# Optimization experiments

Measured on AMD Instinct MI355X. Metric: run time of the kernel, lower is better.

## Reference

```python
import jax, jax.numpy as jnp
import numpy as np

B, N, E, H, ID = 32, 256, 512, 8, 8
D = E // H  # head dim = 64


def setup_inputs() -> dict:
    key = jax.random.key(0)
    ks = jax.random.split(key, 6)
    s = lambda k, shape, fan_in: jax.random.normal(k, shape, jnp.float32) * (fan_in ** -0.5)
    return {
        "x": jax.random.normal(ks[0], (B, N, E), jnp.float32),
        "U": jax.random.normal(ks[1], (B, N, N, ID), jnp.float32),
        "w_qkv": s(ks[2], (3 * E, E), E),   # nn.MultiheadAttention in_proj_weight
        "b_qkv": jnp.zeros((3 * E,), jnp.float32),
        "w_out": s(ks[3], (E, E), E),       # out_proj.weight
        "b_out": jnp.zeros((E,), jnp.float32),
        "w_u": s(ks[4], (H, ID), ID),       # u_proj.weight
        "b_u": jnp.zeros((H,), jnp.float32),
    }


def reference(x, U, w_qkv, b_qkv, w_out, b_out, w_u, b_u):
    # fused QKV projection (torch MHA uses a single in_proj)
    qkv = x @ w_qkv.T + b_qkv                      # [B,N,3E]
    q, k, v = jnp.split(qkv, 3, axis=-1)
    split_heads = lambda t: t.reshape(B, N, H, D).transpose(0, 2, 1, 3)  # [B,H,N,D]
    q, k, v = split_heads(q), split_heads(k), split_heads(v)
    # interaction tensor -> one additive bias per head: [B,N,N,H] -> [B,H,N,N]
    bias = (U @ w_u.T + b_u).transpose(0, 3, 1, 2)
    logits = jnp.einsum('bhnd,bhmd->bhnm', q, k) * (D ** -0.5) + bias  # [B,H,N,N]
    attn = jax.nn.softmax(logits, axis=-1)
    o = jnp.einsum('bhnm,bhmd->bhnd', attn, v)     # [B,H,N,D]
    o = o.transpose(0, 2, 1, 3).reshape(B, N, E)
    return o @ w_out.T + b_out
```

## Files before the change

### kernel.cpp

```cpp
#include <hip/hip_runtime.h>
#include <stdint.h>

#define Bn 32
#define Nn 256
#define En 512
#define Hn 8
#define Dn 64

typedef __attribute__((ext_vector_type(8))) short bf16x8;
typedef __attribute__((ext_vector_type(4))) short bf16x4;
typedef __attribute__((ext_vector_type(4))) float f32x4;
typedef __attribute__((ext_vector_type(4))) _Float16 h4f;

__device__ __forceinline__ unsigned short f2bf(float f){
  union{float f; uint32_t i;} v; v.f = f;
  uint32_t i = v.i;
  return (unsigned short)((i + 0x7fffu + ((i>>16)&1u)) >> 16);
}

__device__ __forceinline__ void stage16(const unsigned short* g,
                                        unsigned short* lds_wave_base,
                                        unsigned short* lds_lane){
#if __has_builtin(__builtin_amdgcn_global_load_lds)
  __builtin_amdgcn_global_load_lds(
      (const __attribute__((address_space(1))) unsigned int*)g,
      (__attribute__((address_space(3))) unsigned int*)lds_wave_base, 16, 0, 0);
  (void)lds_lane;
#else
  *(bf16x8*)lds_lane = *(const bf16x8*)g;
  (void)lds_wave_base;
#endif
}

__global__ __launch_bounds__(256) void convert_x(
    const float* __restrict__ x, unsigned short* __restrict__ xb){
  size_t i = ((size_t)blockIdx.x * 256 + threadIdx.x) * 8;
  float4 a = *(const float4*)(x + i);
  float4 b = *(const float4*)(x + i + 4);
  bf16x8 p;
  p[0]=(short)f2bf(a.x); p[1]=(short)f2bf(a.y); p[2]=(short)f2bf(a.z); p[3]=(short)f2bf(a.w);
  p[4]=(short)f2bf(b.x); p[5]=(short)f2bf(b.y); p[6]=(short)f2bf(b.z); p[7]=(short)f2bf(b.w);
  *(bf16x8*)(xb + i) = p;
}

__global__ __launch_bounds__(256) void prep_kernel(
    const float* __restrict__ x, unsigned short* __restrict__ xb,
    const float* __restrict__ U, const float* __restrict__ w_u,
    const float* __restrict__ b_u, unsigned short* __restrict__ bias16,
    const float* __restrict__ wq, unsigned short* __restrict__ wqb,
    const float* __restrict__ wo, unsigned short* __restrict__ wob){
  __shared__ float s_wu[64];
  __shared__ float s_bu[8];
  const int bx = blockIdx.x;
  const int tid = threadIdx.x;
  if (bx < 2048 || bx >= 4096) {
    const float* src; unsigned short* dst; size_t i;
    if (bx < 2048)      { src = x;  dst = xb;  i = ((size_t)bx * 256 + tid) * 8; }
    else if (bx < 4480) { src = wq; dst = wqb; i = ((size_t)(bx-4096) * 256 + tid) * 8; }
    else                { src = wo; dst = wob; i = ((size_t)(bx-4480) * 256 + tid) * 8; }
    float4 a = *(const float4*)(src + i);
    float4 b = *(const float4*)(src + i + 4);
    bf16x8 p;
    p[0]=(short)f2bf(a.x); p[1]=(short)f2bf(a.y); p[2]=(short)f2bf(a.z); p[3]=(short)f2bf(a.w);
    p[4]=(short)f2bf(b.x); p[5]=(short)f2bf(b.y); p[6]=(short)f2bf(b.z); p[7]=(short)f2bf(b.w);
    *(bf16x8*)(dst + i) = p;
    return;
  }
  if (tid < 64) s_wu[tid] = w_u[tid];
  if (tid < 8)  s_bu[tid] = b_u[tid];
  __syncthreads();
  const int t  = (bx - 2048) * 256 + tid;
  const int m_ = t & 255;
  const int n4 = (t >> 8) & 63;
  const int bb = t >> 14;
  const float* up = U + ((size_t)(bb*Nn + n4*4)*Nn + m_) * 8;
  float u[4][8];
  #pragma unroll
  for (int r = 0; r < 4; ++r) {
    float4 a = *(const float4*)(up + (size_t)r * (Nn*8));
    float4 c = *(const float4*)(up + (size_t)r * (Nn*8) + 4);
    u[r][0]=a.x; u[r][1]=a.y; u[r][2]=a.z; u[r][3]=a.w;
    u[r][4]=c.x; u[r][5]=c.y; u[r][6]=c.z; u[r][7]=c.w;
  }
  const int    lane_in = ((n4 & 3) * 16 + (m_ & 15)) * 4;
  const size_t tbase   = ((size_t)(n4 >> 2) * 16 + (m_ >> 4)) * 256;
  #pragma unroll
  for (int h = 0; h < 8; ++h) {
    const float bu = s_bu[h];
    float acc[4];
    #pragma unroll
    for (int r = 0; r < 4; ++r) {
      float a = bu;
      #pragma unroll
      for (int id = 0; id < 8; ++id) a += u[r][id] * s_wu[h*8 + id];
      acc[r] = a;
    }
    h4f hv;
    hv[0]=(_Float16)acc[0]; hv[1]=(_Float16)acc[1];
    hv[2]=(_Float16)acc[2]; hv[3]=(_Float16)acc[3];
    *(h4f*)(bias16 + (size_t)(bb*Hn + h) * 65536 + tbase + lane_in) = hv;
  }
}

__global__ __launch_bounds__(256) void qkv_gemm3(
    const unsigned short* __restrict__ xb, const unsigned short* __restrict__ wqb,
    const float* __restrict__ bq,
    unsigned short* __restrict__ q_ws, unsigned short* __restrict__ k_ws,
    unsigned short* __restrict__ v_ws){
  __shared__ unsigned short s_a[2][128*64];
  __shared__ unsigned short s_b[2][128*64];
  const int tid = threadIdx.x;
  const int bx = blockIdx.x;
  const int by = blockIdx.y;
  const int row0 = by * 128, n0 = bx * 128;
  const int lane = tid & 63, wv = tid >> 6;
  const int wr = wv >> 1, wc = wv & 1;
  const int lm = lane & 15, quad = lane >> 4;
  f32x4 acc[4][4] = {};

  auto stage_tile = [&](int buf, int kc){
    const int k0 = kc * 64;
    #pragma unroll
    for (int i = 0; i < 4; ++i) {
      const int ci = i*256 + tid;
      const int r = ci >> 3, c = ci & 7;
      const int sc = (c ^ (r & 7)) * 8;
      stage16(xb  + (size_t)(row0 + r)*512 + k0 + sc,
              s_a[buf] + (size_t)(i*256 + wv*64)*8, s_a[buf] + (size_t)ci*8);
      stage16(wqb + (size_t)(n0  + r)*512 + k0 + sc,
              s_b[buf] + (size_t)(i*256 + wv*64)*8, s_b[buf] + (size_t)ci*8);
    }
  };

  stage_tile(0, 0);
  __syncthreads();
  #pragma unroll 1
  for (int kc = 0; kc < 8; ++kc) {
    const int cur = kc & 1;
    if (kc + 1 < 8) stage_tile(cur ^ 1, kc + 1);
    #pragma unroll
    for (int ks = 0; ks < 2; ++ks) {
      bf16x8 af[4], bfr[4];
      #pragma unroll
      for (int mt = 0; mt < 4; ++mt) {
        const int r = wr*64 + mt*16 + lm;
        af[mt] = *(const bf16x8*)(s_a[cur] + (size_t)r*64 + (((ks*4 + quad) ^ (r & 7)) * 8));
      }
      #pragma unroll
      for (int nt = 0; nt < 4; ++nt) {
        const int r = wc*64 + nt*16 + lm;
        bfr[nt] = *(const bf16x8*)(s_b[cur] + (size_t)r*64 + (((ks*4 + quad) ^ (r & 7)) * 8));
      }
      #pragma unroll
      for (int mt = 0; mt < 4; ++mt)
        #pragma unroll
        for (int nt = 0; nt < 4; ++nt)
          acc[mt][nt] = __builtin_amdgcn_mfma_f32_16x16x32_bf16(af[mt], bfr[nt], acc[mt][nt], 0, 0, 0);
    }
    __syncthreads();
  }
  #pragma unroll
  for (int nt = 0; nt < 4; ++nt) {
    int c = n0 + wc*64 + nt*16 + lm;
    float bias = bq[c];
    int sec = c >> 9, ch = c & 511, h = ch >> 6, d = ch & 63;
    #pragma unroll
    for (int mt = 0; mt < 4; ++mt) {
      #pragma unroll
      for (int r = 0; r < 4; ++r) {
        int grow = row0 + wr*64 + mt*16 + quad*4 + r;
        int b = grow >> 8, n = grow & 255;
        float val = acc[mt][nt][r] + bias;
        if (sec == 0)      q_ws[(((size_t)b*Hn + h)*Nn + n)*Dn + d] = f2bf(val * 0.125f);
        else if (sec == 1) k_ws[(((size_t)b*Hn + h)*Nn + n)*Dn + d] = f2bf(val);
        else               v_ws[(((size_t)b*Hn + h)*Dn + d)*Nn + n] = f2bf(val);
      }
    }
  }
}

__global__ __launch_bounds__(256) void oproj_gemm3(
    const unsigned short* __restrict__ o_ws, const unsigned short* __restrict__ wob,
    const float* __restrict__ bo, float* __restrict__ out){
  __shared__ unsigned short s_a[2][128*64];
  __shared__ unsigned short s_b[2][64*64];
  const int tid = threadIdx.x;
  const int bx = blockIdx.x;
  const int by = blockIdx.y;
  const int row0 = by * 128, n0 = bx * 64;
  const int lane = tid & 63, wv = tid >> 6;
  const int wr = wv >> 1, wc = wv & 1;
  const int lm = lane & 15, quad = lane >> 4;
  f32x4 acc[4][2] = {};

  auto stage_tile = [&](int buf, int kc){
    const int k0 = kc * 64;
    #pragma unroll
    for (int i = 0; i < 4; ++i) {
      const int ci = i*256 + tid;
      const int r = ci >> 3, c = ci & 7;
      const int sc = (c ^ (r & 7)) * 8;
      stage16(o_ws + (size_t)(row0 + r)*512 + k0 + sc,
              s_a[buf] + (size_t)(i*256 + wv*64)*8, s_a[buf] + (size_t)ci*8);
    }
    #pragma unroll
    for (int i = 0; i < 2; ++i) {
      const int ci = i*256 + tid;
      const int r = ci >> 3, c = ci & 7;
      const int sc = (c ^ (r & 7)) * 8;
      stage16(wob + (size_t)(n0 + r)*512 + k0 + sc,
              s_b[buf] + (size_t)(i*256 + wv*64)*8, s_b[buf] + (size_t)ci*8);
    }
  };

  stage_tile(0, 0);
  __syncthreads();
  #pragma unroll 1
  for (int kc = 0; kc < 8; ++kc) {
    const int cur = kc & 1;
    if (kc + 1 < 8) stage_tile(cur ^ 1, kc + 1);
    #pragma unroll
    for (int ks = 0; ks < 2; ++ks) {
      bf16x8 af[4], bfr[2];
      #pragma unroll
      for (int mt = 0; mt < 4; ++mt) {
        const int r = wr*64 + mt*16 + lm;
        af[mt] = *(const bf16x8*)(s_a[cur] + (size_t)r*64 + (((ks*4 + quad) ^ (r & 7)) * 8));
      }
      #pragma unroll
      for (int nt = 0; nt < 2; ++nt) {
        const int r = wc*32 + nt*16 + lm;
        bfr[nt] = *(const bf16x8*)(s_b[cur] + (size_t)r*64 + (((ks*4 + quad) ^ (r & 7)) * 8));
      }
      #pragma unroll
      for (int mt = 0; mt < 4; ++mt)
        #pragma unroll
        for (int nt = 0; nt < 2; ++nt)
          acc[mt][nt] = __builtin_amdgcn_mfma_f32_16x16x32_bf16(af[mt], bfr[nt], acc[mt][nt], 0, 0, 0);
    }
    __syncthreads();
  }
  #pragma unroll
  for (int nt = 0; nt < 2; ++nt) {
    int c = n0 + wc*32 + nt*16 + lm;
    float bias = bo[c];
    #pragma unroll
    for (int mt = 0; mt < 4; ++mt)
      #pragma unroll
      for (int r = 0; r < 4; ++r) {
        int grow = row0 + wr*64 + mt*16 + quad*4 + r;
        out[(size_t)grow*512 + c] = acc[mt][nt][r] + bias;
      }
  }
}

__global__ __launch_bounds__(256) void attn_fast(
    const unsigned short* __restrict__ bias16,
    const unsigned short* __restrict__ q_ws, const unsigned short* __restrict__ k_ws,
    const unsigned short* __restrict__ v_ws, unsigned short* __restrict__ o_ws){
  __shared__ unsigned short s_p[4][16][40];
  const int tid = threadIdx.x;
  const int wv = tid >> 6, lane = tid & 63;
  const int lm = lane & 15, quad = lane >> 4;
  const int bx = blockIdx.x;
  const int g  = (bx & 7) * 8 + ((bx >> 3) >> 4);
  const int qt = (bx >> 3) & 15;
  const int b = g >> 1, hp = g & 1;
  const int h = hp * 4 + wv;
  const size_t hb = (size_t)b * Hn + h;
  const int qt0 = qt * 16;
  const unsigned short* qp = q_ws + (hb*Nn + qt0 + lm) * Dn;
  const bf16x8 qa0 = *(const bf16x8*)(qp + quad*8);
  const bf16x8 qa1 = *(const bf16x8*)(qp + 32 + quad*8);
  const unsigned short* bt = bias16 + (hb*16 + qt) * 16 * 256 + (size_t)lane*4;
  f32x4 oa[4] = {};
  float m0[4], l0[4];
  #pragma unroll
  for (int r = 0; r < 4; ++r) { m0[r] = -3.0e38f; l0[r] = 0.f; }
  #pragma unroll 1
  for (int ck = 0; ck < 8; ++ck) {
    f32x4 la0, la1;
    #pragma unroll
    for (int t = 0; t < 2; ++t) {
      const int key0 = ck*32 + t*16;
      const h4f hv = *(const h4f*)(bt + (ck*2 + t) * 256);
      f32x4 c0;
      #pragma unroll
      for (int r = 0; r < 4; ++r) c0[r] = (float)hv[r];
      const unsigned short* kp = k_ws + (hb*Nn + key0 + lm) * Dn;
      c0 = __builtin_amdgcn_mfma_f32_16x16x32_bf16(qa0, *(const bf16x8*)(kp + quad*8),      c0, 0, 0, 0);
      c0 = __builtin_amdgcn_mfma_f32_16x16x32_bf16(qa1, *(const bf16x8*)(kp + 32 + quad*8), c0, 0, 0, 0);
      if (t == 0) la0 = c0; else la1 = c0;
    }
    #pragma unroll
    for (int r = 0; r < 4; ++r) {
      float tm = fmaxf(la0[r], la1[r]);
      #pragma unroll
      for (int msk = 1; msk < 16; msk <<= 1) tm = fmaxf(tm, __shfl_xor(tm, msk));
      float mn = fmaxf(m0[r], tm);
      float al = __expf(m0[r] - mn);
      m0[r] = mn;
      float e0 = __expf(la0[r] - mn), e1 = __expf(la1[r] - mn);
      la0[r] = e0; la1[r] = e1;
      float s = e0 + e1;
      #pragma unroll
      for (int msk = 1; msk < 16; msk <<= 1) s += __shfl_xor(s, msk);
      l0[r] = l0[r] * al + s;
      #pragma unroll
      for (int nt = 0; nt < 4; ++nt) oa[nt][r] *= al;
    }
    #pragma unroll
    for (int r = 0; r < 4; ++r) {
      s_p[wv][quad*4+r][lm]      = f2bf(la0[r]);
      s_p[wv][quad*4+r][16 + lm] = f2bf(la1[r]);
    }
    const bf16x8 ap = *(const bf16x8*)&s_p[wv][lm][quad*8];
    #pragma unroll
    for (int nt = 0; nt < 4; ++nt) {
      const bf16x8 bv = *(const bf16x8*)(v_ws + (hb*Dn + nt*16 + lm)*Nn + ck*32 + quad*8);
      oa[nt] = __builtin_amdgcn_mfma_f32_16x16x32_bf16(ap, bv, oa[nt], 0, 0, 0);
    }
  }
  #pragma unroll
  for (int r = 0; r < 4; ++r) {
    const float inv = 1.0f / l0[r];
    const int n = qt0 + quad*4 + r;
    #pragma unroll
    for (int nt = 0; nt < 4; ++nt)
      o_ws[((size_t)(b*Nn + n))*En + h*64 + nt*16 + lm] = f2bf(oa[nt][r] * inv);
  }
}

__global__ __launch_bounds__(256) void qkv_gemm(
    const unsigned short* __restrict__ xb, const float* __restrict__ wq,
    const float* __restrict__ bq,
    unsigned short* __restrict__ q_ws, unsigned short* __restrict__ k_ws,
    unsigned short* __restrict__ v_ws){
  __shared__ unsigned short s_a[128][40];
  __shared__ unsigned short s_b[128][40];
  const int tid = threadIdx.x;
  const int bx = blockIdx.x;
  const int by = blockIdx.y;
  const int row0 = by * 128, n0 = bx * 128;
  const int lane = tid & 63, wv = tid >> 6;
  const int wr = wv >> 1, wc = wv & 1;
  const int lm = lane & 15, quad = lane >> 4;
  const int sr = tid >> 3, sc4 = (tid & 7) * 4;
  f32x4 acc[4][4] = {};
  for (int kc = 0; kc < 16; ++kc) {
    const int k0 = kc * 32;
    __syncthreads();
    #pragma unroll
    for (int i = 0; i < 2; ++i) {
      int g = tid * 2 + i;
      int r = g >> 2, c8 = (g & 3) * 8;
      *(bf16x8*)&s_a[r][c8] = *(const bf16x8*)(xb + (size_t)(row0 + r)*512 + k0 + c8);
    }
    #pragma unroll
    for (int i = 0; i < 4; ++i) {
      int r = sr + i * 32;
      float4 vb = *(const float4*)(wq + (size_t)(n0 + r) * 512 + k0 + sc4);
      bf16x4 pb;
      pb[0]=(short)f2bf(vb.x); pb[1]=(short)f2bf(vb.y); pb[2]=(short)f2bf(vb.z); pb[3]=(short)f2bf(vb.w);
      *(bf16x4*)&s_b[r][sc4] = pb;
    }
    __syncthreads();
    bf16x8 af[4], bfr[4];
    #pragma unroll
    for (int mt = 0; mt < 4; ++mt) af[mt]  = *(const bf16x8*)&s_a[wr*64 + mt*16 + lm][quad*8];
    #pragma unroll
    for (int nt = 0; nt < 4; ++nt) bfr[nt] = *(const bf16x8*)&s_b[wc*64 + nt*16 + lm][quad*8];
    #pragma unroll
    for (int mt = 0; mt < 4; ++mt)
      #pragma unroll
      for (int nt = 0; nt < 4; ++nt)
        acc[mt][nt] = __builtin_amdgcn_mfma_f32_16x16x32_bf16(af[mt], bfr[nt], acc[mt][nt], 0, 0, 0);
  }
  #pragma unroll
  for (int nt = 0; nt < 4; ++nt) {
    int c = n0 + wc*64 + nt*16 + lm;
    float bias = bq[c];
    int sec = c >> 9, ch = c & 511, h = ch >> 6, d = ch & 63;
    #pragma unroll
    for (int mt = 0; mt < 4; ++mt) {
      #pragma unroll
      for (int r = 0; r < 4; ++r) {
        int grow = row0 + wr*64 + mt*16 + quad*4 + r;
        int b = grow >> 8, n = grow & 255;
        float val = acc[mt][nt][r] + bias;
        if (sec == 0)      q_ws[(((size_t)b*Hn + h)*Nn + n)*Dn + d] = f2bf(val * 0.125f);
        else if (sec == 1) k_ws[(((size_t)b*Hn + h)*Nn + n)*Dn + d] = f2bf(val);
        else               v_ws[(((size_t)b*Hn + h)*Dn + d)*Nn + n] = f2bf(val);
      }
    }
  }
}

__global__ __launch_bounds__(256) void attn_kernel(
    const float* __restrict__ U, const float* __restrict__ w_u, const float* __restrict__ b_u,
    const unsigned short* __restrict__ q_ws, const unsigned short* __restrict__ k_ws,
    const unsigned short* __restrict__ v_ws, unsigned short* __restrict__ o_ws){
  __shared__ unsigned short s_p[4][2][16][40];
  __shared__ float s_wu[64];
  __shared__ float s_bu[8];
  const int tid = threadIdx.x;
  const int wv = tid >> 6, lane = tid & 63;
  const int lm = lane & 15, quad = lane >> 4;
  const int blk = blockIdx.x;
  const int b = blk >> 4, qt0 = (blk & 15) * 16;
  if (tid < 64) s_wu[tid] = w_u[tid];
  if (tid < 8)  s_bu[tid] = b_u[tid];
  __syncthreads();
  const int h0 = wv * 2, h1 = h0 + 1;
  const size_t hb0 = (size_t)b * Hn + h0, hb1 = hb0 + 1;
  float wu0[8], wu1[8];
  #pragma unroll
  for (int i = 0; i < 8; ++i) { wu0[i] = s_wu[h0*8 + i]; wu1[i] = s_wu[h1*8 + i]; }
  const float bu0 = s_bu[h0], bu1 = s_bu[h1];
  const unsigned short* q0p = q_ws + (hb0*Nn + qt0 + lm)*Dn;
  const unsigned short* q1p = q_ws + (hb1*Nn + qt0 + lm)*Dn;
  const bf16x8 qa0 = *(const bf16x8*)(q0p + quad*8);
  const bf16x8 qa1 = *(const bf16x8*)(q0p + 32 + quad*8);
  const bf16x8 qb0 = *(const bf16x8*)(q1p + quad*8);
  const bf16x8 qb1 = *(const bf16x8*)(q1p + 32 + quad*8);
  f32x4 oa[4] = {}, ob[4] = {};
  float m0[4], m1[4], l0[4], l1[4];
  #pragma unroll
  for (int r = 0; r < 4; ++r) { m0[r] = m1[r] = -3.0e38f; l0[r] = l1[r] = 0.f; }
  const float* Ub = U + ((size_t)(b*Nn + qt0)) * Nn * 8;
  #pragma unroll 1
  for (int ck = 0; ck < 8; ++ck) {
    f32x4 la0, la1, lb0, lb1;
    #pragma unroll
    for (int t = 0; t < 2; ++t) {
      const int key0 = ck*32 + t*16;
      f32x4 c0, c1;
      #pragma unroll
      for (int r = 0; r < 4; ++r) {
        const float4* up = (const float4*)(Ub + ((size_t)(quad*4+r)*Nn + key0 + lm)*8);
        float4 ua = up[0], uc = up[1];
        c0[r] = bu0 + ua.x*wu0[0] + ua.y*wu0[1] + ua.z*wu0[2] + ua.w*wu0[3]
                    + uc.x*wu0[4] + uc.y*wu0[5] + uc.z*wu0[6] + uc.w*wu0[7];
        c1[r] = bu1 + ua.x*wu1[0] + ua.y*wu1[1] + ua.z*wu1[2] + ua.w*wu1[3]
                    + uc.x*wu1[4] + uc.y*wu1[5] + uc.z*wu1[6] + uc.w*wu1[7];
      }
      const unsigned short* k0p = k_ws + (hb0*Nn + key0 + lm)*Dn;
      const unsigned short* k1p = k_ws + (hb1*Nn + key0 + lm)*Dn;
      bf16x8 kf;
      kf = *(const bf16x8*)(k0p + quad*8);
      c0 = __builtin_amdgcn_mfma_f32_16x16x32_bf16(qa0, kf, c0, 0, 0, 0);
      kf = *(const bf16x8*)(k0p + 32 + quad*8);
      c0 = __builtin_amdgcn_mfma_f32_16x16x32_bf16(qa1, kf, c0, 0, 0, 0);
      kf = *(const bf16x8*)(k1p + quad*8);
      c1 = __builtin_amdgcn_mfma_f32_16x16x32_bf16(qb0, kf, c1, 0, 0, 0);
      kf = *(const bf16x8*)(k1p + 32 + quad*8);
      c1 = __builtin_amdgcn_mfma_f32_16x16x32_bf16(qb1, kf, c1, 0, 0, 0);
      if (t == 0) { la0 = c0; lb0 = c1; } else { la1 = c0; lb1 = c1; }
    }
    #pragma unroll
    for (int r = 0; r < 4; ++r) {
      {
        float tm = fmaxf(la0[r], la1[r]);
        #pragma unroll
        for (int msk = 1; msk < 16; msk <<= 1) tm = fmaxf(tm, __shfl_xor(tm, msk));
        float mn = fmaxf(m0[r], tm);
        float al = __expf(m0[r] - mn);
        m0[r] = mn;
        float e0 = __expf(la0[r] - mn), e1 = __expf(la1[r] - mn);
        la0[r] = e0; la1[r] = e1;
        float s = e0 + e1;
        #pragma unroll
        for (int msk = 1; msk < 16; msk <<= 1) s += __shfl_xor(s, msk);
        l0[r] = l0[r] * al + s;
        #pragma unroll
        for (int nt = 0; nt < 4; ++nt) oa[nt][r] *= al;
      }
      {
        float tm = fmaxf(lb0[r], lb1[r]);
        #pragma unroll
        for (int msk = 1; msk < 16; msk <<= 1) tm = fmaxf(tm, __shfl_xor(tm, msk));
        float mn = fmaxf(m1[r], tm);
        float al = __expf(m1[r] - mn);
        m1[r] = mn;
        float e0 = __expf(lb0[r] - mn), e1 = __expf(lb1[r] - mn);
        lb0[r] = e0; lb1[r] = e1;
        float s = e0 + e1;
        #pragma unroll
        for (int msk = 1; msk < 16; msk <<= 1) s += __shfl_xor(s, msk);
        l1[r] = l1[r] * al + s;
        #pragma unroll
        for (int nt = 0; nt < 4; ++nt) ob[nt][r] *= al;
      }
    }
    #pragma unroll
    for (int r = 0; r < 4; ++r) {
      s_p[wv][0][quad*4+r][lm]      = f2bf(la0[r]);
      s_p[wv][0][quad*4+r][16 + lm] = f2bf(la1[r]);
      s_p[wv][1][quad*4+r][lm]      = f2bf(lb0[r]);
      s_p[wv][1][quad*4+r][16 + lm] = f2bf(lb1[r]);
    }
    const bf16x8 ap0 = *(const bf16x8*)&s_p[wv][0][lm][quad*8];
    const bf16x8 ap1 = *(const bf16x8*)&s_p[wv][1][lm][quad*8];
    #pragma unroll
    for (int nt = 0; nt < 4; ++nt) {
      bf16x8 bv = *(const bf16x8*)(v_ws + (hb0*Dn + nt*16 + lm)*Nn + ck*32 + quad*8);
      oa[nt] = __builtin_amdgcn_mfma_f32_16x16x32_bf16(ap0, bv, oa[nt], 0, 0, 0);
      bv = *(const bf16x8*)(v_ws + (hb1*Dn + nt*16 + lm)*Nn + ck*32 + quad*8);
      ob[nt] = __builtin_amdgcn_mfma_f32_16x16x32_bf16(ap1, bv, ob[nt], 0, 0, 0);
    }
  }
  #pragma unroll
  for (int r = 0; r < 4; ++r) {
    const float i0 = 1.0f / l0[r], i1 = 1.0f / l1[r];
    const int n = qt0 + quad*4 + r;
    #pragma unroll
    for (int nt = 0; nt < 4; ++nt) {
      o_ws[((size_t)(b*Nn + n))*En + h0*64 + nt*16 + lm] = f2bf(oa[nt][r] * i0);
      o_ws[((size_t)(b*Nn + n))*En + h1*64 + nt*16 + lm] = f2bf(ob[nt][r] * i1);
    }
  }
}

__global__ __launch_bounds__(256) void oproj_gemm(
    const unsigned short* __restrict__ o_ws, const float* __restrict__ wo,
    const float* __restrict__ bo, float* __restrict__ out){
  __shared__ unsigned short s_a[128][40];
  __shared__ unsigned short s_b[128][40];
  const int tid = threadIdx.x;
  const int bx = blockIdx.x;
  const int by = blockIdx.y;
  const int row0 = by * 128, n0 = bx * 128;
  const int lane = tid & 63, wv = tid >> 6;
  const int wr = wv >> 1, wc = wv & 1;
  const int lm = lane & 15, quad = lane >> 4;
  const int sr = tid >> 3, sc4 = (tid & 7) * 4;
  f32x4 acc[4][4] = {};
  for (int kc = 0; kc < 16; ++kc) {
    const int k0 = kc * 32;
    __syncthreads();
    #pragma unroll
    for (int i = 0; i < 2; ++i) {
      int g = tid * 2 + i;
      int r = g >> 2, c8 = (g & 3) * 8;
      *(bf16x8*)&s_a[r][c8] = *(const bf16x8*)(o_ws + (size_t)(row0 + r)*512 + k0 + c8);
    }
    #pragma unroll
    for (int i = 0; i < 4; ++i) {
      int r = sr + i * 32;
      float4 vb = *(const float4*)(wo + (size_t)(n0 + r) * 512 + k0 + sc4);
      bf16x4 pb;
      pb[0]=(short)f2bf(vb.x); pb[1]=(short)f2bf(vb.y); pb[2]=(short)f2bf(vb.z); pb[3]=(short)f2bf(vb.w);
      *(bf16x4*)&s_b[r][sc4] = pb;
    }
    __syncthreads();
    bf16x8 af[4], bfr[4];
    #pragma unroll
    for (int mt = 0; mt < 4; ++mt) af[mt]  = *(const bf16x8*)&s_a[wr*64 + mt*16 + lm][quad*8];
    #pragma unroll
    for (int nt = 0; nt < 4; ++nt) bfr[nt] = *(const bf16x8*)&s_b[wc*64 + nt*16 + lm][quad*8];
    #pragma unroll
    for (int mt = 0; mt < 4; ++mt)
      #pragma unroll
      for (int nt = 0; nt < 4; ++nt)
        acc[mt][nt] = __builtin_amdgcn_mfma_f32_16x16x32_bf16(af[mt], bfr[nt], acc[mt][nt], 0, 0, 0);
  }
  #pragma unroll
  for (int nt = 0; nt < 4; ++nt) {
    int c = n0 + wc*64 + nt*16 + lm;
    float bias = bo[c];
    #pragma unroll
    for (int mt = 0; mt < 4; ++mt)
      #pragma unroll
      for (int r = 0; r < 4; ++r) {
        int grow = row0 + wr*64 + mt*16 + quad*4 + r;
        out[(size_t)grow*512 + c] = acc[mt][nt][r] + bias;
      }
  }
}

extern "C" void kernel_launch(void* const* d_in, const int* in_sizes, int n_in,
                              void* d_out, int out_size, void* d_ws, size_t ws_size,
                              hipStream_t stream) {
  const float* x     = (const float*)d_in[0];
  const float* U     = (const float*)d_in[1];
  const float* w_qkv = (const float*)d_in[2];
  const float* b_qkv = (const float*)d_in[3];
  const float* w_out = (const float*)d_in[4];
  const float* b_out = (const float*)d_in[5];
  const float* w_u   = (const float*)d_in[6];
  const float* b_u   = (const float*)d_in[7];
  float* out = (float*)d_out;

  const size_t per = (size_t)Bn * Hn * Nn * Dn;
  unsigned short* q_ws = (unsigned short*)d_ws;
  unsigned short* k_ws = q_ws + per;
  unsigned short* v_ws = k_ws + per;
  unsigned short* o_ws = v_ws + per;
  unsigned short* bias16 = o_ws + per;
  unsigned short* wqb = bias16 + (size_t)Bn*Hn*Nn*Nn;
  unsigned short* wob = wqb + (size_t)3*En*En;

  const size_t need = (per*4 + (size_t)Bn*Hn*Nn*Nn + (size_t)3*En*En + (size_t)En*En) * 2;

  if (ws_size >= need) {
    prep_kernel<<<dim3(4608),  dim3(256), 0, stream>>>(x, o_ws, U, w_u, b_u, bias16,
                                                       w_qkv, wqb, w_out, wob);
    qkv_gemm3 <<<dim3(12, 64), dim3(256), 0, stream>>>(o_ws, wqb, b_qkv, q_ws, k_ws, v_ws);
    attn_fast <<<dim3(1024),   dim3(256), 0, stream>>>(bias16, q_ws, k_ws, v_ws, o_ws);
    oproj_gemm3<<<dim3(8, 64), dim3(256), 0, stream>>>(o_ws, wob, b_out, out);
  } else {
    convert_x <<<dim3(2048),  dim3(256), 0, stream>>>(x, o_ws);
    qkv_gemm  <<<dim3(12, 64), dim3(256), 0, stream>>>(o_ws, w_qkv, b_qkv, q_ws, k_ws, v_ws);
    attn_kernel<<<dim3(Bn * 16), dim3(256), 0, stream>>>(U, w_u, b_u, q_ws, k_ws, v_ws, o_ws);
    oproj_gemm<<<dim3(4, 64), dim3(256), 0, stream>>>(o_ws, w_out, b_out, out);
  }
}
```

Baseline: 214.5 us.

## Use vmcnt-based prefetch waits and stage QKV epilogue through LDS

Both projection GEMMs replace __syncthreads with an explicit s_waitcnt vmcnt on the async global-to-LDS loads followed by a raw s_barrier. Only the current tile must land while the next tile's loads stay in flight, which aims to overlap loading with MFMA work. The QKV GEMM epilogue now writes results into a padded LDS tile, transposed for V, and then emits vectorized 4-element bf16 stores. This replaces scattered 2-byte global stores, especially the strided V-transposed writes. The risk is that the vmcnt counts must match the number of staged loads exactly, or the kernel reads stale LDS data.

Result: faster. 197.8 us (-7.8%).

```diff
diff --git a/kernel.cpp b/kernel.cpp
--- a/kernel.cpp
+++ b/kernel.cpp
@@ -102,13 +102,12 @@
   }
 }
 
-__global__ __launch_bounds__(256) void qkv_gemm3(
+__global__ __launch_bounds__(256) void qkv_gemm4(
     const unsigned short* __restrict__ xb, const unsigned short* __restrict__ wqb,
     const float* __restrict__ bq,
     unsigned short* __restrict__ q_ws, unsigned short* __restrict__ k_ws,
     unsigned short* __restrict__ v_ws){
-  __shared__ unsigned short s_a[2][128*64];
-  __shared__ unsigned short s_b[2][128*64];
+  __shared__ unsigned short smem[32768];
   const int tid = threadIdx.x;
   const int bx = blockIdx.x;
   const int by = blockIdx.y;
@@ -120,36 +119,46 @@
 
   auto stage_tile = [&](int buf, int kc){
     const int k0 = kc * 64;
+    unsigned short* sa = smem + buf * 8192;
+    unsigned short* sb = smem + 16384 + buf * 8192;
     #pragma unroll
     for (int i = 0; i < 4; ++i) {
       const int ci = i*256 + tid;
       const int r = ci >> 3, c = ci & 7;
       const int sc = (c ^ (r & 7)) * 8;
       stage16(xb  + (size_t)(row0 + r)*512 + k0 + sc,
-              s_a[buf] + (size_t)(i*256 + wv*64)*8, s_a[buf] + (size_t)ci*8);
+              sa + (size_t)(i*256 + wv*64)*8, sa + (size_t)ci*8);
       stage16(wqb + (size_t)(n0  + r)*512 + k0 + sc,
-              s_b[buf] + (size_t)(i*256 + wv*64)*8, s_b[buf] + (size_t)ci*8);
+              sb + (size_t)(i*256 + wv*64)*8, sb + (size_t)ci*8);
     }
   };
 
   stage_tile(0, 0);
-  __syncthreads();
   #pragma unroll 1
   for (int kc = 0; kc < 8; ++kc) {
     const int cur = kc & 1;
-    if (kc + 1 < 8) stage_tile(cur ^ 1, kc + 1);
+    if (kc < 7) {
+      stage_tile(cur ^ 1, kc + 1);
+      asm volatile("s_waitcnt vmcnt(8)" ::: "memory");
+    } else {
+      asm volatile("s_waitcnt vmcnt(0)" ::: "memory");
+    }
+    __builtin_amdgcn_s_barrier();
+    __builtin_amdgcn_sched_barrier(0);
+    const unsigned short* sa = smem + cur * 8192;
+    const unsigned short* sb = smem + 16384 + cur * 8192;
     #pragma unroll
     for (int ks = 0; ks < 2; ++ks) {
       bf16x8 af[4], bfr[4];
       #pragma unroll
       for (int mt = 0; mt < 4; ++mt) {
         const int r = wr*64 + mt*16 + lm;
-        af[mt] = *(const bf16x8*)(s_a[cur] + (size_t)r*64 + (((ks*4 + quad) ^ (r & 7)) * 8));
+        af[mt] = *(const bf16x8*)(sa + (size_t)r*64 + (((ks*4 + quad) ^ (r & 7)) * 8));
       }
       #pragma unroll
       for (int nt = 0; nt < 4; ++nt) {
         const int r = wc*64 + nt*16 + lm;
-        bfr[nt] = *(const bf16x8*)(s_b[cur] + (size_t)r*64 + (((ks*4 + quad) ^ (r & 7)) * 8));
+        bfr[nt] = *(const bf16x8*)(sb + (size_t)r*64 + (((ks*4 + quad) ^ (r & 7)) * 8));
       }
       #pragma unroll
       for (int mt = 0; mt < 4; ++mt)
@@ -157,33 +166,70 @@
         for (int nt = 0; nt < 4; ++nt)
           acc[mt][nt] = __builtin_amdgcn_mfma_f32_16x16x32_bf16(af[mt], bfr[nt], acc[mt][nt], 0, 0, 0);
     }
-    __syncthreads();
-  }
-  #pragma unroll
-  for (int nt = 0; nt < 4; ++nt) {
-    int c = n0 + wc*64 + nt*16 + lm;
-    float bias = bq[c];
-    int sec = c >> 9, ch = c & 511, h = ch >> 6, d = ch & 63;
-    #pragma unroll
-    for (int mt = 0; mt < 4; ++mt) {
-      #pragma unroll
-      for (int r = 0; r < 4; ++r) {
-        int grow = row0 + wr*64 + mt*16 + quad*4 + r;
-        int b = grow >> 8, n = grow & 255;
-        float val = acc[mt][nt][r] + bias;
-        if (sec == 0)      q_ws[(((size_t)b*Hn + h)*Nn + n)*Dn + d] = f2bf(val * 0.125f);
-        else if (sec == 1) k_ws[(((size_t)b*Hn + h)*Nn + n)*Dn + d] = f2bf(val);
-        else               v_ws[(((size_t)b*Hn + h)*Dn + d)*Nn + n] = f2bf(val);
-      }
-    }
-  }
-}
-
-__global__ __launch_bounds__(256) void oproj_gemm3(
+    __builtin_amdgcn_sched_barrier(0);
+    __builtin_amdgcn_s_barrier();
+  }
+
+  const int sec = bx >> 2;
+  float bias[4];
+  #pragma unroll
+  for (int nt = 0; nt < 4; ++nt) bias[nt] = bq[n0 + wc*64 + nt*16 + lm];
+  unsigned short* tile = smem;
+  if (sec < 2) {
+    const float scale = (sec == 0) ? 0.125f : 1.0f;
+    #pragma unroll
+    for (int nt = 0; nt < 4; ++nt) {
+      const int col = wc*64 + nt*16 + lm;
+      #pragma unroll
+      for (int mt = 0; mt < 4; ++mt)
+        #pragma unroll
+        for (int r = 0; r < 4; ++r) {
+          const int row = wr*64 + mt*16 + quad*4 + r;
+          tile[row*136 + col] = f2bf((acc[mt][nt][r] + bias[nt]) * scale);
+        }
+    }
+  } else {
+    #pragma unroll
+    for (int nt = 0; nt < 4; ++nt) {
+      const int col = wc*64 + nt*16 + lm;
+      #pragma unroll
+      for (int mt = 0; mt < 4; ++mt)
+        #pragma unroll
+        for (int r = 0; r < 4; ++r) {
+          const int row = wr*64 + mt*16 + quad*4 + r;
+          tile[col*136 + row] = f2bf(acc[mt][nt][r] + bias[nt]);
+        }
+    }
+  }
+  __syncthreads();
+  if (sec < 2) {
+    unsigned short* dst = (sec == 0) ? q_ws : k_ws;
+    #pragma unroll
+    for (int it = 0; it < 16; ++it) {
+      const int rown = it*8 + (tid >> 5);
+      const int col  = (tid & 31) * 4;
+      bf16x4 vv = *(const bf16x4*)(tile + rown*136 + col);
+      const int c = n0 + col, ch = c & 511, h = ch >> 6, d = ch & 63;
+      const int grow = row0 + rown, b = grow >> 8, n = grow & 255;
+      *(bf16x4*)(dst + (((size_t)b*Hn + h)*Nn + n)*Dn + d) = vv;
+    }
+  } else {
+    const int b = row0 >> 8, nbase = row0 & 255;
+    #pragma unroll
+    for (int it = 0; it < 16; ++it) {
+      const int c  = it*8 + (tid >> 5);
+      const int n4 = (tid & 31) * 4;
+      bf16x4 vv = *(const bf16x4*)(tile + c*136 + n4);
+      const int ch = (n0 - 1024) + c, h = ch >> 6, d = ch & 63;
+      *(bf16x4*)(v_ws + (((size_t)b*Hn + h)*Dn + d)*Nn + nbase + n4) = vv;
+    }
+  }
+}
+
+__global__ __launch_bounds__(256) void oproj_gemm4(
     const unsigned short* __restrict__ o_ws, const unsigned short* __restrict__ wob,
     const float* __restrict__ bo, float* __restrict__ out){
-  __shared__ unsigned short s_a[2][128*64];
-  __shared__ unsigned short s_b[2][64*64];
+  __shared__ unsigned short smem[24576];
   const int tid = threadIdx.x;
   const int bx = blockIdx.x;
   const int by = blockIdx.y;
@@ -195,13 +241,15 @@
 
   auto stage_tile = [&](int buf, int kc){
     const int k0 = kc * 64;
+    unsigned short* sa = smem + buf * 8192;
+    unsigned short* sb = smem + 16384 + buf * 4096;
     #pragma unroll
     for (int i = 0; i < 4; ++i) {
       const int ci = i*256 + tid;
       const int r = ci >> 3, c = ci & 7;
       const int sc = (c ^ (r & 7)) * 8;
       stage16(o_ws + (size_t)(row0 + r)*512 + k0 + sc,
-              s_a[buf] + (size_t)(i*256 + wv*64)*8, s_a[buf] + (size_t)ci*8);
+              sa + (size_t)(i*256 + wv*64)*8, sa + (size_t)ci*8);
     }
     #pragma unroll
     for (int i = 0; i < 2; ++i) {
@@ -209,28 +257,36 @@
       const int r = ci >> 3, c = ci & 7;
       const int sc = (c ^ (r & 7)) * 8;
       stage16(wob + (size_t)(n0 + r)*512 + k0 + sc,
-              s_b[buf] + (size_t)(i*256 + wv*64)*8, s_b[buf] + (size_t)ci*8);
+              sb + (size_t)(i*256 + wv*64)*8, sb + (size_t)ci*8);
     }
   };
 
   stage_tile(0, 0);
-  __syncthreads();
   #pragma unroll 1
   for (int kc = 0; kc < 8; ++kc) {
     const int cur = kc & 1;
-    if (kc + 1 < 8) stage_tile(cur ^ 1, kc + 1);
+    if (kc < 7) {
+      stage_tile(cur ^ 1, kc + 1);
+      asm volatile("s_waitcnt vmcnt(6)" ::: "memory");
+    } else {
+      asm volatile("s_waitcnt vmcnt(0)" ::: "memory");
+    }
+    __builtin_amdgcn_s_barrier();
+    __builtin_amdgcn_sched_barrier(0);
+    const unsigned short* sa = smem + cur * 8192;
+    const unsigned short* sb = smem + 16384 + cur * 4096;
     #pragma unroll
     for (int ks = 0; ks < 2; ++ks) {
       bf16x8 af[4], bfr[2];
       #pragma unroll
       for (int mt = 0; mt < 4; ++mt) {
         const int r = wr*64 + mt*16 + lm;
-        af[mt] = *(const bf16x8*)(s_a[cur] + (size_t)r*64 + (((ks*4 + quad) ^ (r & 7)) * 8));
+        af[mt] = *(const bf16x8*)(sa + (size_t)r*64 + (((ks*4 + quad) ^ (r & 7)) * 8));
       }
       #pragma unroll
       for (int nt = 0; nt < 2; ++nt) {
         const int r = wc*32 + nt*16 + lm;
-        bfr[nt] = *(const bf16x8*)(s_b[cur] + (size_t)r*64 + (((ks*4 + quad) ^ (r & 7)) * 8));
+        bfr[nt] = *(const bf16x8*)(sb + (size_t)r*64 + (((ks*4 + quad) ^ (r & 7)) * 8));
       }
       #pragma unroll
       for (int mt = 0; mt < 4; ++mt)
@@ -238,7 +294,8 @@
         for (int nt = 0; nt < 2; ++nt)
           acc[mt][nt] = __builtin_amdgcn_mfma_f32_16x16x32_bf16(af[mt], bfr[nt], acc[mt][nt], 0, 0, 0);
     }
-    __syncthreads();
+    __builtin_amdgcn_sched_barrier(0);
+    __builtin_amdgcn_s_barrier();
   }
   #pragma unroll
   for (int nt = 0; nt < 2; ++nt) {
@@ -605,9 +662,9 @@
   if (ws_size >= need) {
     prep_kernel<<<dim3(4608),  dim3(256), 0, stream>>>(x, o_ws, U, w_u, b_u, bias16,
                                                        w_qkv, wqb, w_out, wob);
-    qkv_gemm3 <<<dim3(12, 64), dim3(256), 0, stream>>>(o_ws, wqb, b_qkv, q_ws, k_ws, v_ws);
+    qkv_gemm4 <<<dim3(12, 64), dim3(256), 0, stream>>>(o_ws, wqb, b_qkv, q_ws, k_ws, v_ws);
     attn_fast <<<dim3(1024),   dim3(256), 0, stream>>>(bias16, q_ws, k_ws, v_ws, o_ws);
-    oproj_gemm3<<<dim3(8, 64), dim3(256), 0, stream>>>(o_ws, wob, b_out, out);
+    oproj_gemm4<<<dim3(8, 64), dim3(256), 0, stream>>>(o_ws, wob, b_out, out);
   } else {
     convert_x <<<dim3(2048),  dim3(256), 0, stream>>>(x, o_ws);
     qkv_gemm  <<<dim3(12, 64), dim3(256), 0, stream>>>(o_ws, w_qkv, b_qkv, q_ws, k_ws, v_ws);
```
